# Kernel optimization log

Measured on AMD Instinct MI355X. Metric: run time of the kernel, lower is better.

Reference implementation:

```python
import jax, jax.numpy as jnp
import numpy as np

N = 50000   # nodes
E = 625000  # edges
H = 128     # hidden
B = 32      # bottleneck_dim


def _layernorm(x, g, b, eps=1e-5):
    m = jnp.mean(x, axis=-1, keepdims=True)
    v = jnp.var(x, axis=-1, keepdims=True)
    return (x - m) * jax.lax.rsqrt(v + eps) * g + b


def setup_inputs() -> dict:
    key = jax.random.key(0)
    ks = jax.random.split(key, 16)
    s = 0.05
    return {
        "x": jax.random.normal(ks[0], (N, H), dtype=jnp.float32),
        "edge_index": jax.random.randint(ks[1], (2, E), 0, N, dtype=jnp.int64),
        # down GINConv (eps trainable, init 0) + its bottleneck MLP
        "eps_down": jnp.zeros((), jnp.float32),
        "dw1": jax.random.normal(ks[2], (H, B), dtype=jnp.float32) * s,
        "dg1": jnp.ones((B,), jnp.float32),
        "db1": jnp.zeros((B,), jnp.float32),
        "dw2": jax.random.normal(ks[3], (B, H), dtype=jnp.float32) * s,
        # up GINConv
        "eps_up": jnp.zeros((), jnp.float32),
        "uw1": jax.random.normal(ks[4], (H, B), dtype=jnp.float32) * s,
        "ug1": jnp.ones((B,), jnp.float32),
        "ub1": jnp.zeros((B,), jnp.float32),
        "uw2": jax.random.normal(ks[5], (B, H), dtype=jnp.float32) * s,
        # outer LayerNorms
        "ln1_g": jnp.ones((H,), jnp.float32),
        "ln1_b": jnp.zeros((H,), jnp.float32),
        "ln2_g": jnp.ones((H,), jnp.float32),
        "ln2_b": jnp.zeros((H,), jnp.float32),
        # direction embeddings [2, H]
        "dir_emb": jax.random.normal(ks[6], (2, H), dtype=jnp.float32) * 0.02,
        # combine Linear(2H -> H) with bias
        "cw": jax.random.normal(ks[7], (2 * H, H), dtype=jnp.float32) * s,
        "cb": jnp.zeros((H,), jnp.float32),
    }


def reference(x, edge_index, eps_down, dw1, dg1, db1, dw2,
              eps_up, uw1, ug1, ub1, uw2,
              ln1_g, ln1_b, ln2_g, ln2_b, dir_emb, cw, cb):
    src, dst = edge_index[0], edge_index[1]

    def gin(s_idx, d_idx, eps, w1, g1, b1, w2):
        # scatter-add of source features onto destination nodes
        agg = jax.ops.segment_sum(x[s_idx], d_idx, num_segments=N)  # [N, H]
        h = (1.0 + eps) * x + agg
        # bottleneck MLP: Linear -> LayerNorm -> ReLU -> (Dropout=id) -> Linear
        h = _layernorm(h @ w1, g1, b1)
        return jax.nn.relu(h) @ w2  # [N, H]

    h_down = _layernorm(jax.nn.relu(gin(src, dst, eps_down, dw1, dg1, db1, dw2) + dir_emb[0]), ln1_g, ln1_b)
    # reversed edges for the "up" direction
    h_up = _layernorm(jax.nn.relu(gin(dst, src, eps_up, uw1, ug1, ub1, uw2) + dir_emb[1]), ln2_g, ln2_b)

    h_cat = jnp.concatenate([h_down, h_up], axis=-1)  # [N, 2H]
    return h_cat @ cw + cb  # [N, H]
```

## Files before the change

### kernel.cpp

```cpp
#include <hip/hip_runtime.h>

#define N_NODES 50000
#define NPAD 50048
#define N_EDGES 625000
#define H 128
#define B 32
#define PSTRIDE 40
#define CAP 64
#define NPART 8
#define ROWS_PER_PART (2 * N_NODES / NPART)
#define NGRP 3125
#define FILLB (2443 * NPART)

using bf16x8  = __attribute__((ext_vector_type(8))) short;
using f32x4   = __attribute__((ext_vector_type(4))) float;
using u16x4   = __attribute__((ext_vector_type(4))) unsigned short;

static __device__ __forceinline__ unsigned short f2bf(float f) {
    unsigned u = __float_as_uint(f);
    unsigned r = (u + 0x7fff + ((u >> 16) & 1)) >> 16;
    return (unsigned short)r;
}
static __device__ __forceinline__ float bf2f(unsigned short h) {
    return __uint_as_float(((unsigned)h) << 16);
}

__global__ __launch_bounds__(256) void fill_convert_kernel(
    const int* __restrict__ ei, int* __restrict__ cursor,
    unsigned short* __restrict__ bucket,
    const float* __restrict__ x, unsigned* __restrict__ xb,
    const float* __restrict__ dw1, const float* __restrict__ uw1,
    const float* __restrict__ dw2, const float* __restrict__ uw2,
    const float* __restrict__ cw,
    unsigned short* __restrict__ w1h, unsigned short* __restrict__ w1l,
    unsigned short* __restrict__ w2h, unsigned short* __restrict__ w2l,
    unsigned short* __restrict__ cwh)
{
    int b = blockIdx.x;
    if (b < FILLB) {
        int p  = b & 7;
        int eb = b >> 3;
        int e = eb * 256 + threadIdx.x;
        if (e >= N_EDGES) return;
        int lo = p * ROWS_PER_PART, hi = lo + ROWS_PER_PART;
        int s = ei[e];
        int d = ei[N_EDGES + e];
        int r2 = N_NODES + s;
        if (d >= lo && d < hi) {
            int pos = atomicAdd(&cursor[d], 1);
            if (pos < CAP) bucket[(size_t)d * CAP + pos] = (unsigned short)s;
        }
        if (r2 >= lo && r2 < hi) {
            int pos = atomicAdd(&cursor[r2], 1);
            if (pos < CAP) bucket[(size_t)r2 * CAP + pos] = (unsigned short)d;
        }
        return;
    }
    b -= FILLB;
    if (b < 12500) {
        int i = b * 256 + threadIdx.x;
        float2 v = ((const float2*)x)[i];
        xb[i] = ((unsigned)f2bf(v.y) << 16) | f2bf(v.x);
        return;
    }
    int i = (b - 12500) * 256 + threadIdx.x;
    if (i < 8192) {
        int j = i & 4095;
        int c = j >> 7, k = j & 127;
        const float* src = (i >> 12) ? uw1 : dw1;
        float v = src[k * 32 + c];
        unsigned short h = f2bf(v);
        w1h[i] = h; w1l[i] = f2bf(v - bf2f(h));
    } else if (i < 16384) {
        int j = i - 8192;
        int jj = j & 4095;
        int c = jj >> 5, k = jj & 31;
        const float* src = (j >> 12) ? uw2 : dw2;
        float v = src[k * 128 + c];
        unsigned short h = f2bf(v);
        w2h[j] = h; w2l[j] = f2bf(v - bf2f(h));
    } else {
        int j = i - 16384;
        int c = j >> 8, k = j & 255;
        cwh[j] = f2bf(cw[k * 128 + c]);
    }
}

__global__ __launch_bounds__(256) void y_gemm_kernel(
    const unsigned short* __restrict__ xbu,
    const unsigned short* __restrict__ w1bT_hi, const unsigned short* __restrict__ w1bT_lo,
    unsigned short* __restrict__ y)
{
    int w = threadIdx.x >> 6, lane = threadIdx.x & 63;
    int l15 = lane & 15, g = lane >> 4;
    int blk = blockIdx.x;
    int dir = (blk >= 782) ? 1 : 0;
    int r0 = (blk - dir * 782) * 64 + w * 16;

    const unsigned short* wh = w1bT_hi + dir * 4096;
    const unsigned short* wl = w1bT_lo + dir * 4096;

    int node = r0 + l15; if (node >= N_NODES) node = N_NODES - 1;
    const unsigned short* xrow = xbu + (size_t)node * H;

    f32x4 acc[2];
    acc[0] = (f32x4){0.f,0.f,0.f,0.f};
    acc[1] = (f32x4){0.f,0.f,0.f,0.f};
    #pragma unroll
    for (int ks = 0; ks < 4; ++ks) {
        int ko = ks * 32 + g * 8;
        bf16x8 bh = *(const bf16x8*)(xrow + ko);
        #pragma unroll
        for (int t = 0; t < 2; ++t) {
            bf16x8 ah = *(const bf16x8*)(wh + (t * 16 + l15) * H + ko);
            bf16x8 al = *(const bf16x8*)(wl + (t * 16 + l15) * H + ko);
            acc[t] = __builtin_amdgcn_mfma_f32_16x16x32_bf16(ah, bh, acc[t], 0, 0, 0);
            acc[t] = __builtin_amdgcn_mfma_f32_16x16x32_bf16(al, bh, acc[t], 0, 0, 0);
        }
    }

    unsigned short* orow = y + ((size_t)dir * NPAD + r0 + l15) * B;
    #pragma unroll
    for (int t = 0; t < 2; ++t) {
        u16x4 o = {f2bf(acc[t][0]), f2bf(acc[t][1]), f2bf(acc[t][2]), f2bf(acc[t][3])};
        *(u16x4*)(orow + t * 16 + g * 4) = o;
    }
}

__global__ __launch_bounds__(256) void gather_mlp_kernel(
    const unsigned* __restrict__ y,
    const int* __restrict__ cursor, const unsigned short* __restrict__ bucket,
    const float* __restrict__ eps_d_p, const float* __restrict__ eps_u_p,
    const unsigned short* __restrict__ w2bT_hi, const unsigned short* __restrict__ w2bT_lo,
    const float* __restrict__ dg1, const float* __restrict__ db1,
    const float* __restrict__ ug1, const float* __restrict__ ub1,
    const float* __restrict__ ln1g, const float* __restrict__ ln1b,
    const float* __restrict__ ln2g, const float* __restrict__ ln2b,
    const float* __restrict__ dir_emb,
    unsigned short* __restrict__ hcat)
{
    __shared__ unsigned short plds[4][2][16 * PSTRIDE];

    int w = threadIdx.x >> 6, lane = threadIdx.x & 63;
    int sgrp = lane >> 4, l16 = lane & 15;
    int blk = blockIdx.x;
    int dir = (blk >= 782) ? 1 : 0;
    int r0 = (blk - dir * 782) * 64 + w * 16;

    float eps = 1.f + (dir ? eps_u_p[0] : eps_d_p[0]);
    const unsigned* yu = y + (size_t)dir * NPAD * 16;

    const float* g1p = dir ? ug1 : dg1;
    const float* b1p = dir ? ub1 : db1;
    float2 gv = ((const float2*)g1p)[l16];
    float2 bv = ((const float2*)b1p)[l16];

    unsigned short* mh = &plds[w][0][0];
    unsigned short* ml = &plds[w][1][0];

    for (int p = 0; p < 4; ++p) {
        int rloc = p * 4 + sgrp;
        int node = r0 + rloc;
        float p0 = 0.f, p1 = 0.f;
        if (node < N_NODES) {
            int ridx = dir * N_NODES + node;
            int deg = cursor[ridx]; if (deg > CAP) deg = CAP;
            const unsigned short* nb = bucket + (size_t)ridx * CAP;
            float a0 = 0.f, a1 = 0.f;
            for (int base = 0; base < deg; base += 16) {
                int m = deg - base; if (m > 16) m = 16;
                int id = (l16 < m) ? (int)nb[base + l16] : 0;
                int lim = m - 1;
                for (int j = 0; j < m; j += 8) {
                    unsigned r[8];
                    #pragma unroll
                    for (int q = 0; q < 8; ++q) {
                        int idx = j + q; if (idx > lim) idx = lim;
                        int nbid = __shfl(id, (sgrp << 4) + idx);
                        r[q] = yu[nbid * 16 + l16];
                    }
                    #pragma unroll
                    for (int q = 0; q < 8; ++q) {
                        if (j + q <= lim) {
                            a0 += __uint_as_float(r[q] << 16);
                            a1 += __uint_as_float(r[q] & 0xffff0000u);
                        }
                    }
                }
            }
            unsigned sv = yu[node * 16 + l16];
            float c0 = eps * __uint_as_float(sv << 16) + a0;
            float c1 = eps * __uint_as_float(sv & 0xffff0000u) + a1;
            float ss = c0 + c1, s2 = c0 * c0 + c1 * c1;
            #pragma unroll
            for (int m2 = 1; m2 <= 8; m2 <<= 1) {
                ss += __shfl_xor(ss, m2);
                s2 += __shfl_xor(s2, m2);
            }
            float mean = ss * (1.f / 32.f);
            float var  = s2 * (1.f / 32.f) - mean * mean;
            float rs   = rsqrtf(var + 1e-5f);
            p0 = fmaxf((c0 - mean) * rs * gv.x + bv.x, 0.f);
            p1 = fmaxf((c1 - mean) * rs * gv.y + bv.y, 0.f);
        }
        unsigned short q0 = f2bf(p0), q1 = f2bf(p1);
        *(unsigned*)(mh + rloc * PSTRIDE + 2 * l16) = ((unsigned)q1 << 16) | q0;
        *(unsigned*)(ml + rloc * PSTRIDE + 2 * l16) =
            ((unsigned)f2bf(p1 - bf2f(q1)) << 16) | f2bf(p0 - bf2f(q0));
    }

    int l15 = lane & 15, g = lane >> 4;

    const unsigned short* w2h = w2bT_hi + dir * 4096;
    const unsigned short* w2l = w2bT_lo + dir * 4096;

    bf16x8 pbh = *(const bf16x8*)(mh + l15 * PSTRIDE + g * 8);
    bf16x8 pbl = *(const bf16x8*)(ml + l15 * PSTRIDE + g * 8);

    f32x4 acc2[8];
    #pragma unroll
    for (int t = 0; t < 8; ++t) acc2[t] = (f32x4){0.f,0.f,0.f,0.f};
    #pragma unroll
    for (int t = 0; t < 8; ++t) {
        bf16x8 ah = *(const bf16x8*)(w2h + (t * 16 + l15) * 32 + g * 8);
        bf16x8 al = *(const bf16x8*)(w2l + (t * 16 + l15) * 32 + g * 8);
        acc2[t] = __builtin_amdgcn_mfma_f32_16x16x32_bf16(ah, pbh, acc2[t], 0, 0, 0);
        acc2[t] = __builtin_amdgcn_mfma_f32_16x16x32_bf16(al, pbh, acc2[t], 0, 0, 0);
        acc2[t] = __builtin_amdgcn_mfma_f32_16x16x32_bf16(ah, pbl, acc2[t], 0, 0, 0);
    }

    float av[8][4];
    float u = 0.f, u2 = 0.f;
    #pragma unroll
    for (int t = 0; t < 8; ++t) {
        float4 de = *(const float4*)(dir_emb + dir * H + t * 16 + g * 4);
        av[t][0] = fmaxf(acc2[t][0] + de.x, 0.f);
        av[t][1] = fmaxf(acc2[t][1] + de.y, 0.f);
        av[t][2] = fmaxf(acc2[t][2] + de.z, 0.f);
        av[t][3] = fmaxf(acc2[t][3] + de.w, 0.f);
        #pragma unroll
        for (int r = 0; r < 4; ++r) { u += av[t][r]; u2 += av[t][r] * av[t][r]; }
    }
    u  += __shfl_xor(u, 16);  u  += __shfl_xor(u, 32);
    u2 += __shfl_xor(u2, 16); u2 += __shfl_xor(u2, 32);
    float m2  = u * (1.f / 128.f);
    float v2  = u2 * (1.f / 128.f) - m2 * m2;
    float rs2 = rsqrtf(v2 + 1e-5f);

    const float* lgp = dir ? ln2g : ln1g;
    const float* lbp = dir ? ln2b : ln1b;
    if ((r0 + l15) < N_NODES) {
        unsigned short* orow = hcat + (size_t)(r0 + l15) * 256 + dir * 128;
        #pragma unroll
        for (int t = 0; t < 8; ++t) {
            float4 gg = *(const float4*)(lgp + t * 16 + g * 4);
            float4 bb = *(const float4*)(lbp + t * 16 + g * 4);
            u16x4 o;
            o[0] = f2bf((av[t][0] - m2) * rs2 * gg.x + bb.x);
            o[1] = f2bf((av[t][1] - m2) * rs2 * gg.y + bb.y);
            o[2] = f2bf((av[t][2] - m2) * rs2 * gg.z + bb.z);
            o[3] = f2bf((av[t][3] - m2) * rs2 * gg.w + bb.w);
            *(u16x4*)(orow + t * 16 + g * 4) = o;
        }
    }
}

__global__ __launch_bounds__(256) void combine_mfma(
    const unsigned short* __restrict__ hcat,
    const unsigned short* __restrict__ cwh,
    const float* __restrict__ cb, float* __restrict__ out)
{
    int w = threadIdx.x >> 6, lane = threadIdx.x & 63;
    int l15 = lane & 15, g = lane >> 4;
    int gid = blockIdx.x * 4 + w;
    int q = gid & 3;
    int j = gid >> 2;

    const unsigned short* abase = cwh + (size_t)(q * 32 + l15) * 256 + g * 8;
    bf16x8 Ah[2][8];
    #pragma unroll
    for (int t = 0; t < 2; ++t)
        #pragma unroll
        for (int ks = 0; ks < 8; ++ks)
            Ah[t][ks] = *(const bf16x8*)(abase + (t * 16) * 256 + ks * 32);

    int grp[4]; int ng = 0;
    #pragma unroll
    for (int k = 0; k < 4; ++k) {
        int gg = j + 782 * k;
        if (gg < NGRP) grp[ng++] = gg;
    }
    if (ng == 0) return;

    bf16x8 Bc[8], Bn[8];
    {
        const unsigned short* bb = hcat + (size_t)grp[0] * 16 * 256 + l15 * 256 + g * 8;
        #pragma unroll
        for (int ks = 0; ks < 8; ++ks) Bc[ks] = *(const bf16x8*)(bb + ks * 32);
    }

    float4 bias0 = *(const float4*)(cb + q * 32 + g * 4);
    float4 bias1 = *(const float4*)(cb + q * 32 + 16 + g * 4);

    for (int i = 0; i < ng; ++i) {
        if (i + 1 < ng) {
            const unsigned short* bb = hcat + (size_t)grp[i + 1] * 16 * 256 + l15 * 256 + g * 8;
            #pragma unroll
            for (int ks = 0; ks < 8; ++ks) Bn[ks] = *(const bf16x8*)(bb + ks * 32);
        }

        f32x4 acc0 = (f32x4){0.f,0.f,0.f,0.f};
        f32x4 acc1 = (f32x4){0.f,0.f,0.f,0.f};
        #pragma unroll
        for (int ks = 0; ks < 8; ++ks) {
            acc0 = __builtin_amdgcn_mfma_f32_16x16x32_bf16(Ah[0][ks], Bc[ks], acc0, 0, 0, 0);
            acc1 = __builtin_amdgcn_mfma_f32_16x16x32_bf16(Ah[1][ks], Bc[ks], acc1, 0, 0, 0);
        }

        float* orow = out + (size_t)(grp[i] * 16 + l15) * 128 + q * 32;
        f32x4 v0 = acc0, v1 = acc1;
        v0[0] += bias0.x; v0[1] += bias0.y; v0[2] += bias0.z; v0[3] += bias0.w;
        v1[0] += bias1.x; v1[1] += bias1.y; v1[2] += bias1.z; v1[3] += bias1.w;
        *(f32x4*)(orow + g * 4) = v0;
        *(f32x4*)(orow + 16 + g * 4) = v1;

        #pragma unroll
        for (int ks = 0; ks < 8; ++ks) Bc[ks] = Bn[ks];
    }
}

extern "C" void kernel_launch(void* const* d_in, const int* in_sizes, int n_in,
                              void* d_out, int out_size, void* d_ws, size_t ws_size,
                              hipStream_t stream) {
    const float* x     = (const float*)d_in[0];
    const int*   ei    = (const int*)d_in[1];
    const float* eps_d = (const float*)d_in[2];
    const float* dw1   = (const float*)d_in[3];
    const float* dg1   = (const float*)d_in[4];
    const float* db1   = (const float*)d_in[5];
    const float* dw2   = (const float*)d_in[6];
    const float* eps_u = (const float*)d_in[7];
    const float* uw1   = (const float*)d_in[8];
    const float* ug1   = (const float*)d_in[9];
    const float* ub1   = (const float*)d_in[10];
    const float* uw2   = (const float*)d_in[11];
    const float* ln1g  = (const float*)d_in[12];
    const float* ln1b  = (const float*)d_in[13];
    const float* ln2g  = (const float*)d_in[14];
    const float* ln2b  = (const float*)d_in[15];
    const float* dire  = (const float*)d_in[16];
    const float* cw    = (const float*)d_in[17];
    const float* cb    = (const float*)d_in[18];

    int* cursor = (int*)d_ws;
    unsigned short* bucket = (unsigned short*)(cursor + 2 * N_NODES);
    unsigned* xb  = (unsigned*)(bucket + (size_t)2 * N_NODES * CAP);
    unsigned short* yarr = (unsigned short*)(xb + (size_t)N_NODES * 64);
    unsigned short* hcat = yarr + (size_t)2 * NPAD * B;
    unsigned short* w1bT_hi = hcat + (size_t)N_NODES * 256;
    unsigned short* w1bT_lo = w1bT_hi + 8192;
    unsigned short* w2bT_hi = w1bT_lo + 8192;
    unsigned short* w2bT_lo = w2bT_hi + 8192;
    unsigned short* cwbT_hi = w2bT_lo + 8192;

    hipMemsetAsync(cursor, 0, 2 * N_NODES * sizeof(int), stream);

    fill_convert_kernel<<<FILLB + 12500 + 192, 256, 0, stream>>>(
        ei, cursor, bucket, x, xb, dw1, uw1, dw2, uw2, cw,
        w1bT_hi, w1bT_lo, w2bT_hi, w2bT_lo, cwbT_hi);

    y_gemm_kernel<<<1564, 256, 0, stream>>>(
        (const unsigned short*)xb, w1bT_hi, w1bT_lo, yarr);

    gather_mlp_kernel<<<1564, 256, 0, stream>>>(
        (const unsigned*)yarr, cursor, bucket, eps_d, eps_u,
        w2bT_hi, w2bT_lo,
        dg1, db1, ug1, ub1, ln1g, ln1b, ln2g, ln2b, dire, hcat);

    combine_mfma<<<782, 256, 0, stream>>>(hcat, cwbT_hi, cb, (float*)d_out);
}
```

Before: 149.7 us.

## Fuse x-projection GEMM into front kernel, converting x and W1 on the fly

Merges the y = x·W1 GEMM into the fill/convert kernel. Each GEMM block converts W1 to hi/lo bf16 into LDS and reads fp32 x directly, converting it in registers, so the intermediate bf16 copy of x and one kernel launch go away. Edge bucket stores become nontemporal. In exchange, every GEMM block redoes the W1 conversion and the fp32 x reads are twice as wide, while the GEMM blocks now share the launch with the atomic-heavy bucket fill.

```diff
diff --git a/kernel.cpp b/kernel.cpp
--- a/kernel.cpp
+++ b/kernel.cpp
@@ -10,6 +10,8 @@
 #define NPART 8
 #define ROWS_PER_PART (2 * N_NODES / NPART)
 #define NGRP 3125
+#define YGB 1564
+#define CVB 160
 #define FILLB (2443 * NPART)
 
 using bf16x8  = __attribute__((ext_vector_type(8))) short;
@@ -25,105 +27,104 @@
     return __uint_as_float(((unsigned)h) << 16);
 }
 
-__global__ __launch_bounds__(256) void fill_convert_kernel(
+__global__ __launch_bounds__(256) void front_kernel(
     const int* __restrict__ ei, int* __restrict__ cursor,
     unsigned short* __restrict__ bucket,
-    const float* __restrict__ x, unsigned* __restrict__ xb,
+    const float* __restrict__ x,
     const float* __restrict__ dw1, const float* __restrict__ uw1,
     const float* __restrict__ dw2, const float* __restrict__ uw2,
     const float* __restrict__ cw,
-    unsigned short* __restrict__ w1h, unsigned short* __restrict__ w1l,
     unsigned short* __restrict__ w2h, unsigned short* __restrict__ w2l,
-    unsigned short* __restrict__ cwh)
-{
-    int b = blockIdx.x;
-    if (b < FILLB) {
-        int p  = b & 7;
-        int eb = b >> 3;
-        int e = eb * 256 + threadIdx.x;
-        if (e >= N_EDGES) return;
-        int lo = p * ROWS_PER_PART, hi = lo + ROWS_PER_PART;
-        int s = ei[e];
-        int d = ei[N_EDGES + e];
-        int r2 = N_NODES + s;
-        if (d >= lo && d < hi) {
-            int pos = atomicAdd(&cursor[d], 1);
-            if (pos < CAP) bucket[(size_t)d * CAP + pos] = (unsigned short)s;
-        }
-        if (r2 >= lo && r2 < hi) {
-            int pos = atomicAdd(&cursor[r2], 1);
-            if (pos < CAP) bucket[(size_t)r2 * CAP + pos] = (unsigned short)d;
-        }
-        return;
-    }
-    b -= FILLB;
-    if (b < 12500) {
-        int i = b * 256 + threadIdx.x;
-        float2 v = ((const float2*)x)[i];
-        xb[i] = ((unsigned)f2bf(v.y) << 16) | f2bf(v.x);
-        return;
-    }
-    int i = (b - 12500) * 256 + threadIdx.x;
-    if (i < 8192) {
-        int j = i & 4095;
-        int c = j >> 7, k = j & 127;
-        const float* src = (i >> 12) ? uw1 : dw1;
-        float v = src[k * 32 + c];
-        unsigned short h = f2bf(v);
-        w1h[i] = h; w1l[i] = f2bf(v - bf2f(h));
-    } else if (i < 16384) {
-        int j = i - 8192;
-        int jj = j & 4095;
-        int c = jj >> 5, k = jj & 31;
-        const float* src = (j >> 12) ? uw2 : dw2;
-        float v = src[k * 128 + c];
-        unsigned short h = f2bf(v);
-        w2h[j] = h; w2l[j] = f2bf(v - bf2f(h));
-    } else {
-        int j = i - 16384;
-        int c = j >> 8, k = j & 255;
-        cwh[j] = f2bf(cw[k * 128 + c]);
-    }
-}
-
-__global__ __launch_bounds__(256) void y_gemm_kernel(
-    const unsigned short* __restrict__ xbu,
-    const unsigned short* __restrict__ w1bT_hi, const unsigned short* __restrict__ w1bT_lo,
+    unsigned short* __restrict__ cwh,
     unsigned short* __restrict__ y)
 {
-    int w = threadIdx.x >> 6, lane = threadIdx.x & 63;
-    int l15 = lane & 15, g = lane >> 4;
-    int blk = blockIdx.x;
-    int dir = (blk >= 782) ? 1 : 0;
-    int r0 = (blk - dir * 782) * 64 + w * 16;
-
-    const unsigned short* wh = w1bT_hi + dir * 4096;
-    const unsigned short* wl = w1bT_lo + dir * 4096;
-
-    int node = r0 + l15; if (node >= N_NODES) node = N_NODES - 1;
-    const unsigned short* xrow = xbu + (size_t)node * H;
-
-    f32x4 acc[2];
-    acc[0] = (f32x4){0.f,0.f,0.f,0.f};
-    acc[1] = (f32x4){0.f,0.f,0.f,0.f};
-    #pragma unroll
-    for (int ks = 0; ks < 4; ++ks) {
-        int ko = ks * 32 + g * 8;
-        bf16x8 bh = *(const bf16x8*)(xrow + ko);
+    __shared__ unsigned short wh_lds[32 * 136];
+    __shared__ unsigned short wl_lds[32 * 136];
+
+    int b = blockIdx.x;
+    if (b < YGB) {
+        int dir = (b >= 782) ? 1 : 0;
+        int r0b = (b - dir * 782) * 64;
+        const float* w1src = dir ? uw1 : dw1;
+        for (int j = threadIdx.x; j < 4096; j += 256) {
+            int k = j >> 5, c = j & 31;
+            float v = w1src[j];
+            unsigned short h = f2bf(v);
+            wh_lds[c * 136 + k] = h;
+            wl_lds[c * 136 + k] = f2bf(v - bf2f(h));
+        }
+        __syncthreads();
+
+        int w = threadIdx.x >> 6, lane = threadIdx.x & 63;
+        int l15 = lane & 15, g = lane >> 4;
+        int r0 = r0b + w * 16;
+        int node = r0 + l15; if (node >= N_NODES) node = N_NODES - 1;
+        const float* xrow = x + (size_t)node * H;
+
+        f32x4 acc[2];
+        acc[0] = (f32x4){0.f,0.f,0.f,0.f};
+        acc[1] = (f32x4){0.f,0.f,0.f,0.f};
+        #pragma unroll
+        for (int ks = 0; ks < 4; ++ks) {
+            int ko = ks * 32 + g * 8;
+            float4 xa = *(const float4*)(xrow + ko);
+            float4 xc = *(const float4*)(xrow + ko + 4);
+            union { bf16x8 v; unsigned short u[8]; } bb;
+            bb.u[0] = f2bf(xa.x); bb.u[1] = f2bf(xa.y);
+            bb.u[2] = f2bf(xa.z); bb.u[3] = f2bf(xa.w);
+            bb.u[4] = f2bf(xc.x); bb.u[5] = f2bf(xc.y);
+            bb.u[6] = f2bf(xc.z); bb.u[7] = f2bf(xc.w);
+            #pragma unroll
+            for (int t = 0; t < 2; ++t) {
+                bf16x8 ah = *(const bf16x8*)(wh_lds + (t * 16 + l15) * 136 + ko);
+                bf16x8 al = *(const bf16x8*)(wl_lds + (t * 16 + l15) * 136 + ko);
+                acc[t] = __builtin_amdgcn_mfma_f32_16x16x32_bf16(ah, bb.v, acc[t], 0, 0, 0);
+                acc[t] = __builtin_amdgcn_mfma_f32_16x16x32_bf16(al, bb.v, acc[t], 0, 0, 0);
+            }
+        }
+
+        unsigned short* orow = y + ((size_t)dir * NPAD + r0 + l15) * B;
         #pragma unroll
         for (int t = 0; t < 2; ++t) {
-            bf16x8 ah = *(const bf16x8*)(wh + (t * 16 + l15) * H + ko);
-            bf16x8 al = *(const bf16x8*)(wl + (t * 16 + l15) * H + ko);
-            acc[t] = __builtin_amdgcn_mfma_f32_16x16x32_bf16(ah, bh, acc[t], 0, 0, 0);
-            acc[t] = __builtin_amdgcn_mfma_f32_16x16x32_bf16(al, bh, acc[t], 0, 0, 0);
-        }
-    }
-
-    unsigned short* orow = y + ((size_t)dir * NPAD + r0 + l15) * B;
-    #pragma unroll
-    for (int t = 0; t < 2; ++t) {
-        u16x4 o = {f2bf(acc[t][0]), f2bf(acc[t][1]), f2bf(acc[t][2]), f2bf(acc[t][3])};
-        *(u16x4*)(orow + t * 16 + g * 4) = o;
+            u16x4 o = {f2bf(acc[t][0]), f2bf(acc[t][1]), f2bf(acc[t][2]), f2bf(acc[t][3])};
+            *(u16x4*)(orow + t * 16 + g * 4) = o;
+        }
+        return;
+    }
+    if (b < YGB + CVB) {
+        int i = (b - YGB) * 256 + threadIdx.x;
+        if (i < 8192) {
+            int j = i & 4095;
+            int c = j >> 5, k = j & 31;
+            const float* src = (i >> 12) ? uw2 : dw2;
+            float v = src[k * 128 + c];
+            unsigned short h = f2bf(v);
+            w2h[i] = h; w2l[i] = f2bf(v - bf2f(h));
+        } else {
+            int j = i - 8192;
+            int c = j >> 8, k = j & 255;
+            cwh[j] = f2bf(cw[k * 128 + c]);
+        }
+        return;
+    }
+    int fb = b - (YGB + CVB);
+    int p  = fb & 7;
+    int eb = fb >> 3;
+    int e = eb * 256 + threadIdx.x;
+    if (e >= N_EDGES) return;
+    int lo = p * ROWS_PER_PART, hi = lo + ROWS_PER_PART;
+    int s = ei[e];
+    int d = ei[N_EDGES + e];
+    int r2 = N_NODES + s;
+    if (d >= lo && d < hi) {
+        int pos = atomicAdd(&cursor[d], 1);
+        if (pos < CAP)
+            __builtin_nontemporal_store((unsigned short)s, bucket + (size_t)d * CAP + pos);
+    }
+    if (r2 >= lo && r2 < hi) {
+        int pos = atomicAdd(&cursor[r2], 1);
+        if (pos < CAP)
+            __builtin_nontemporal_store((unsigned short)d, bucket + (size_t)r2 * CAP + pos);
     }
 }
 
@@ -354,23 +355,17 @@
 
     int* cursor = (int*)d_ws;
     unsigned short* bucket = (unsigned short*)(cursor + 2 * N_NODES);
-    unsigned* xb  = (unsigned*)(bucket + (size_t)2 * N_NODES * CAP);
-    unsigned short* yarr = (unsigned short*)(xb + (size_t)N_NODES * 64);
+    unsigned short* yarr = bucket + (size_t)2 * N_NODES * CAP;
     unsigned short* hcat = yarr + (size_t)2 * NPAD * B;
-    unsigned short* w1bT_hi = hcat + (size_t)N_NODES * 256;
-    unsigned short* w1bT_lo = w1bT_hi + 8192;
-    unsigned short* w2bT_hi = w1bT_lo + 8192;
+    unsigned short* w2bT_hi = hcat + (size_t)N_NODES * 256;
     unsigned short* w2bT_lo = w2bT_hi + 8192;
     unsigned short* cwbT_hi = w2bT_lo + 8192;
 
     hipMemsetAsync(cursor, 0, 2 * N_NODES * sizeof(int), stream);
 
-    fill_convert_kernel<<<FILLB + 12500 + 192, 256, 0, stream>>>(
-        ei, cursor, bucket, x, xb, dw1, uw1, dw2, uw2, cw,
-        w1bT_hi, w1bT_lo, w2bT_hi, w2bT_lo, cwbT_hi);
-
-    y_gemm_kernel<<<1564, 256, 0, stream>>>(
-        (const unsigned short*)xb, w1bT_hi, w1bT_lo, yarr);
+    front_kernel<<<YGB + CVB + FILLB, 256, 0, stream>>>(
+        ei, cursor, bucket, x, dw1, uw1, dw2, uw2, cw,
+        w2bT_hi, w2bT_lo, cwbT_hi, yarr);
 
     gather_mlp_kernel<<<1564, 256, 0, stream>>>(
         (const unsigned*)yarr, cursor, bucket, eps_d, eps_u,
```

Result: faster. 145.8 us (-2.6%).
